# Optimization experiments

Measured on AMD Instinct MI355X. Metric: run time of the kernel, lower is better.

Reference implementation:

```python
import jax, jax.numpy as jnp
import numpy as np

THRESHOLD1 = 1.0
THRESHOLD2 = 1.0


def _conv(x, w, stride, pad):
    return jax.lax.conv_general_dilated(
        x, w, window_strides=(stride, stride),
        padding=((pad, pad), (pad, pad)),
        dimension_numbers=('NCHW', 'OIHW', 'NCHW'))


def _percentiles_1_to_99(t):
    # Faithful to torch: k = 1 + round(0.01*q*(n-1)); kthvalue = k-th smallest.
    # One sort + static gather replaces 99 kthvalue calls.
    flat = jnp.sort(t.reshape(-1))
    n = flat.shape[0]  # static under jit
    ks = np.array([1 + round(0.01 * q * (n - 1)) for q in range(1, 100)], dtype=np.int64)
    return flat[ks - 1]  # [99]


def setup_inputs() -> dict:
    key = jax.random.key(0)
    k1, k2, k3, k4 = jax.random.split(key, 4)
    x = jax.random.normal(k1, (64, 128, 56, 56), jnp.float32)
    # Kaiming-ish scaled conv weights
    w1 = jax.random.normal(k2, (256, 128, 3, 3), jnp.float32) * (2.0 / (128 * 9)) ** 0.5
    w2 = jax.random.normal(k3, (256, 256, 3, 3), jnp.float32) * (2.0 / (256 * 9)) ** 0.5
    w_id = jax.random.normal(k4, (256, 128, 1, 1), jnp.float32) * (2.0 / 128) ** 0.5
    return {"x": x, "w1": w1, "w2": w2, "w_id": w_id}


def reference(x, w1, w2, w_id):
    out1 = _conv(x, w1, 2, 1)                 # conv1: [64,256,28,28]
    a = _percentiles_1_to_99(out1)            # percentiles of UNclamped conv1 output
    out = jnp.clip(out1, 0.0, THRESHOLD1)     # out[out>t1]=t1; out[out<0]=0
    # dropout(p=0.0 / eval) is identity
    out = _conv(out, w2, 1, 1)                # conv2
    out = out + _conv(x, w_id, 2, 0)          # residual via 1x1 stride-2 downsample
    b = _percentiles_1_to_99(out)             # percentiles before second clamp
    out = jnp.clip(out, 0.0, THRESHOLD2)
    return out, a, b
```

## Files before the change

kernel.cpp:

```cpp
#include <hip/hip_runtime.h>

typedef unsigned short ushort_t;
typedef unsigned int uint_t;

using short8 = __attribute__((ext_vector_type(8))) short;
using f32x4  = __attribute__((ext_vector_type(4))) float;

#define N_BATCH   64
#define C_MID     256
#define H_OUT     28
#define W_OUT     28
#define SPATIAL   (H_OUT*W_OUT)
#define OUT_ELEMS (N_BATCH*C_MID*SPATIAL)

#define NBINS 2048
#define BIN_LO (-16.0f)
#define BIN_INV 64.0f
#define BIN_W  0.015625f

#define XT_ROW   (57*128)
#define XT_IMG   (57*57*128)
#define O1_ROW   (30*256)
#define O1_IMG   (30*30*256)

#define WAITVM(n) asm volatile("s_waitcnt vmcnt(" #n ")" ::: "memory")
#define BARRIER() asm volatile("s_barrier" ::: "memory")

__device__ __forceinline__ ushort_t f2bf(float f) {
    uint_t u = __float_as_uint(f);
    u += 0x7FFFu + ((u >> 16) & 1u);
    return (ushort_t)(u >> 16);
}

__device__ __forceinline__ void gll16(const ushort_t* g, void* l) {
    __builtin_amdgcn_global_load_lds(
        (const __attribute__((address_space(1))) unsigned int*)g,
        (__attribute__((address_space(3))) unsigned int*)l, 16, 0, 0);
}

__global__ __launch_bounds__(256) void zwtrans(
    uint_t* __restrict__ xT32, uint_t* __restrict__ o1T32,
    const float* __restrict__ w1, const float* __restrict__ w2,
    const float* __restrict__ wid, ushort_t* __restrict__ wT1,
    ushort_t* __restrict__ wT2, uint_t* __restrict__ hfA,
    uint_t* __restrict__ hfB)
{
    const int bxx = blockIdx.x, y = blockIdx.y, tid = threadIdx.x;
    if (bxx < 87) {
        int i = bxx * 256 + tid;
        int n = y;
        if (i >= 22080) return;
        if (i < 7232) {
            uint_t* base = xT32 + (size_t)n * (XT_IMG / 2);
            if (i < 3648) base[i] = 0;
            else { int j = i - 3648; int r = (j >> 6) + 1;
                   base[r * (XT_ROW / 2) + (j & 63)] = 0; }
        } else {
            int k = i - 7232;
            uint_t* base = o1T32 + (size_t)n * (O1_IMG / 2);
            if (k < 3840) base[k] = 0;
            else if (k < 7680) base[29 * (O1_ROW / 2) + (k - 3840)] = 0;
            else if (k < 11264) { int j = k - 7680; int r = (j >> 7) + 1;
                   base[r * (O1_ROW / 2) + (j & 127)] = 0; }
            else { int j = k - 11264; int r = (j >> 7) + 1;
                   base[r * (O1_ROW / 2) + 29 * 128 + (j & 127)] = 0; }
        }
    } else {
        int idx = ((bxx - 87) * 64 + y) * 256 + tid;
        if (idx < 2048)      hfA[idx] = 0;
        else if (idx < 4096) hfB[idx - 2048] = 0;
        if (idx < 256 * 1152) {
            int co = idx / 1152, k = idx % 1152;
            int g = k >> 7, ci = k & 127;
            wT1[idx] = f2bf(w1[(co * 128 + ci) * 9 + g]);
        }
        if (idx < 256 * 2432) {
            int co = idx / 2432, k = idx % 2432;
            float v;
            if (k < 2304) { int g = k >> 8, ci = k & 255; v = w2[(co * 256 + ci) * 9 + g]; }
            else          { v = wid[co * 128 + (k - 2304)]; }
            wT2[idx] = f2bf(v);
        }
    }
}

__global__ __launch_bounds__(256) void xtrans(
    const float* __restrict__ x, ushort_t* __restrict__ xT)
{
    __shared__ ushort_t t[224 * 130];
    const int tid = threadIdx.x;
    const int g = blockIdx.x, n = blockIdx.y;
    const float* xs = x + ((size_t)n * 128) * 3136 + g * 4 * 56;

    #pragma unroll
    for (int it = 0; it < 28; ++it) {
        int f = it * 256 + tid;
        int ci = f / 56, r4 = f % 56;
        float4 v = *(const float4*)(xs + ci * 3136 + r4 * 4);
        t[(r4 * 4 + 0) * 130 + ci] = f2bf(v.x);
        t[(r4 * 4 + 1) * 130 + ci] = f2bf(v.y);
        t[(r4 * 4 + 2) * 130 + ci] = f2bf(v.z);
        t[(r4 * 4 + 3) * 130 + ci] = f2bf(v.w);
    }
    __syncthreads();
    ushort_t* xo = xT + (size_t)n * XT_IMG + (g * 4 + 1) * XT_ROW + 128;
    for (int it = 0; it < 56; ++it) {
        int f = it * 256 + tid;
        int pos = f >> 6, c2 = f & 63;
        int r = pos / 56, iw = pos % 56;
        uint_t v = *(const uint_t*)&t[pos * 130 + c2 * 2];
        *(uint_t*)(xo + r * XT_ROW + iw * 128 + c2 * 2) = v;
    }
}

__global__ __launch_bounds__(256, 2) void conv1_mfma(
    const ushort_t* __restrict__ xT, const ushort_t* __restrict__ wT1,
    ushort_t* __restrict__ o1T, ushort_t* __restrict__ bh)
{
    const int bx = blockIdx.x;
    const int tid = threadIdx.x;
    const int wv = tid >> 6, lane = tid & 63;
    const int ln = lane & 15, quad = lane >> 4;
    const int n = bx / 7, rg = bx % 7, r0 = rg * 4;

    __shared__ short8 Ald[2 * 1024];
    __shared__ short8 Bp[2304];

    f32x4 acc[4][7];
    #pragma unroll
    for (int a = 0; a < 4; ++a)
        #pragma unroll
        for (int b = 0; b < 7; ++b) acc[a][b] = (f32x4){0.f, 0.f, 0.f, 0.f};

    int drb[7], cl0[7];
    #pragma unroll
    for (int b = 0; b < 7; ++b) {
        int p = b * 16 + ln;
        drb[b] = 2 * (p / 28);
        cl0[b] = p % 28;
    }

    uint_t poff[9];
    #pragma unroll
    for (int i = 0; i < 9; ++i) {
        int slot = (i * 4 + wv) * 64 + lane;
        int s2 = min(slot, 2051);
        int k8 = s2 / 513;
        int rem = s2 - k8 * 513;
        int dr = rem / 57, j = rem - dr * 57;
        int col = (j < 29) ? (2 * j) : (2 * (j - 29) + 1);
        poff[i] = (uint_t)((2 * r0 + dr) * XT_ROW + col * 128 + k8 * 8);
    }
    const uint_t aoff = (uint_t)((wv * 64 + lane) * 1152);

    const ushort_t* xTimg = xT + (size_t)n * XT_IMG;

    auto stageA = [&](int tap, int c, int buf) {
        #pragma unroll
        for (int jj = 0; jj < 4; ++jj)
            gll16(wT1 + aoff + jj * 8 + tap * 128 + c * 32,
                  (char*)Ald + buf * 16384 + (jj * 256 + wv * 64) * 16);
    };

    for (int c = 0; c < 4; ++c) {
        BARRIER();
        #pragma unroll
        for (int i = 0; i < 9; ++i)
            gll16(xTimg + poff[i] + c * 32, (char*)Bp + ((i * 4 + wv) * 64) * 16);
        if (c == 0) stageA(0, 0, 0);
        WAITVM(0);
        BARRIER();

        #pragma unroll
        for (int t = 0; t < 9; ++t) {
            const int st = c * 9 + t;
            const int buf = st & 1;
            if (t < 8)      stageA(t + 1, c, buf ^ 1);
            else if (c < 3) stageA(0, c + 1, buf ^ 1);
            if (c == 3 && t == 8) { WAITVM(0); } else { WAITVM(4); }
            const int kh = t / 3, kw = t - kh * 3;
            short8 af[4], bf[7];
            #pragma unroll
            for (int a = 0; a < 4; ++a)
                af[a] = Ald[buf * 1024 + quad * 256 + wv * 64 + a * 16 + ln];
            #pragma unroll
            for (int b = 0; b < 7; ++b) {
                int dr = drb[b] + kh;
                int j = (kw == 1) ? (29 + cl0[b]) : (cl0[b] + (kw >> 1));
                bf[b] = Bp[quad * 513 + dr * 57 + j];
            }
            __builtin_amdgcn_s_setprio(1);
            #pragma unroll
            for (int a = 0; a < 4; ++a)
                #pragma unroll
                for (int b = 0; b < 7; ++b)
                    acc[a][b] = __builtin_amdgcn_mfma_f32_16x16x32_bf16(
                        af[a], bf[b], acc[a][b], 0, 0, 0);
            __builtin_amdgcn_s_setprio(0);
        }
    }

    __syncthreads();
    uint_t* hist = (uint_t*)Ald;
    for (int i = tid; i < NBINS; i += 256) hist[i] = 0;
    __syncthreads();

    ushort_t* oimg = o1T + (size_t)n * O1_IMG;
    #pragma unroll
    for (int a = 0; a < 4; ++a) {
        int co = wv * 64 + a * 16 + quad * 4;
        #pragma unroll
        for (int b = 0; b < 7; ++b) {
            int p = b * 16 + ln;
            int h = r0 + p / 28, w = p % 28;
            ushort_t pk[4];
            #pragma unroll
            for (int r = 0; r < 4; ++r) {
                float v = acc[a][b][r];
                int bin = (int)((v - BIN_LO) * BIN_INV);
                bin = min(max(bin, 0), NBINS - 1);
                atomicAdd(&hist[bin], 1u);
                pk[r] = f2bf(fminf(fmaxf(v, 0.f), 1.f));
            }
            uint2 u; u.x = (uint_t)pk[0] | ((uint_t)pk[1] << 16);
            u.y = (uint_t)pk[2] | ((uint_t)pk[3] << 16);
            *(uint2*)(oimg + ((h + 1) * 30 + (w + 1)) * 256 + co) = u;
        }
    }

    __syncthreads();
    size_t blin = (size_t)bx * NBINS;
    for (int i = tid; i < NBINS; i += 256) bh[blin + i] = (ushort_t)hist[i];
}

__global__ __launch_bounds__(256, 2) void conv2_mfma(
    const ushort_t* __restrict__ o1T, const ushort_t* __restrict__ xT,
    const ushort_t* __restrict__ wT2, float* __restrict__ fout,
    ushort_t* __restrict__ bh)
{
    const int bx = blockIdx.x;
    const int tid = threadIdx.x;
    const int wv = tid >> 6, lane = tid & 63;
    const int ln = lane & 15, quad = lane >> 4;
    const int n = bx / 7, rg = bx % 7, r0 = rg * 4;

    __shared__ short8 Ald[2 * 1024];
    __shared__ short8 Bp[768];

    f32x4 acc[4][7];
    #pragma unroll
    for (int a = 0; a < 4; ++a)
        #pragma unroll
        for (int b = 0; b < 7; ++b) acc[a][b] = (f32x4){0.f, 0.f, 0.f, 0.f};

    int rwb[7], cl0[7];
    #pragma unroll
    for (int b = 0; b < 7; ++b) {
        int p = b * 16 + ln;
        rwb[b] = (p / 28) * 32;
        cl0[b] = p % 28;
    }

    uint_t po[3];
    #pragma unroll
    for (int jj = 0; jj < 3; ++jj) {
        int f = (wv * 3 + jj) * 64 + lane;
        int ci8 = f / 192, rem = f % 192;
        int dr = rem >> 5, cl = rem & 31;
        po[jj] = (uint_t)((r0 + dr) * O1_ROW + cl * 256 + ci8 * 8);
    }
    uint_t io[2];
    int isl[2];
    #pragma unroll
    for (int jj = 0; jj < 2; ++jj) {
        int i2 = min(wv * 2 + jj, 6);
        isl[jj] = i2;
        int slot = i2 * 64 + lane;
        int ci8 = slot / 112, pos = slot % 112;
        int h = r0 + pos / 28, w = pos % 28;
        io[jj] = (uint_t)(((2 * h + 1) * 57 + (2 * w + 1)) * 128 + ci8 * 8);
    }
    const ushort_t* asrc = wT2 + (size_t)(wv * 64 + lane) * 2432;

    const ushort_t* o1img = o1T + (size_t)n * O1_IMG;
    const ushort_t* xTimg = xT + (size_t)n * XT_IMG;

    auto stageA = [&](int k0, int buf) {
        #pragma unroll
        for (int jj = 0; jj < 4; ++jj)
            gll16(asrc + k0 + jj * 8,
                  (char*)Ald + buf * 16384 + (jj * 256 + wv * 64) * 16);
    };
    auto stageB = [&](int coff) {
        #pragma unroll
        for (int jj = 0; jj < 3; ++jj)
            gll16(o1img + po[jj] + coff, (char*)Bp + (wv * 3 + jj) * 1024);
    };
    auto stageI = [&](int idh) {
        #pragma unroll
        for (int jj = 0; jj < 2; ++jj)
            gll16(xTimg + io[jj] + idh * 32, (char*)Bp + isl[jj] * 1024);
    };

    for (int c = 0; c < 8; ++c) {
        BARRIER();
        stageB(c * 32);
        if (c == 0) stageA(0, 0);
        WAITVM(0);
        BARRIER();

        #pragma unroll
        for (int t = 0; t < 9; ++t) {
            const int st = c * 9 + t;
            const int buf = st & 1;
            if (t < 8)      stageA((t + 1) * 256 + c * 32, buf ^ 1);
            else if (c < 7) stageA(c * 32 + 32, buf ^ 1);
            if (c == 7 && t == 8) { WAITVM(0); } else { WAITVM(4); }
            const int kh = t / 3, kw = t - kh * 3;
            short8 af[4], bf[7];
            #pragma unroll
            for (int a = 0; a < 4; ++a)
                af[a] = Ald[buf * 1024 + quad * 256 + wv * 64 + a * 16 + ln];
            #pragma unroll
            for (int b = 0; b < 7; ++b)
                bf[b] = Bp[quad * 192 + rwb[b] + kh * 32 + cl0[b] + kw];
            __builtin_amdgcn_s_setprio(1);
            #pragma unroll
            for (int a = 0; a < 4; ++a)
                #pragma unroll
                for (int b = 0; b < 7; ++b)
                    acc[a][b] = __builtin_amdgcn_mfma_f32_16x16x32_bf16(
                        af[a], bf[b], acc[a][b], 0, 0, 0);
            __builtin_amdgcn_s_setprio(0);
        }
    }

    #pragma unroll
    for (int idh = 0; idh < 4; ++idh) {
        BARRIER();
        stageI(idh);
        if (idh == 0) stageA(2304, 0);
        WAITVM(0);
        BARRIER();
        if (idh < 3) stageA(2304 + (idh + 1) * 32, (idh + 1) & 1);
        short8 af[4], bf[7];
        #pragma unroll
        for (int a = 0; a < 4; ++a)
            af[a] = Ald[(idh & 1) * 1024 + quad * 256 + wv * 64 + a * 16 + ln];
        #pragma unroll
        for (int b = 0; b < 7; ++b)
            bf[b] = Bp[quad * 112 + b * 16 + ln];
        __builtin_amdgcn_s_setprio(1);
        #pragma unroll
        for (int a = 0; a < 4; ++a)
            #pragma unroll
            for (int b = 0; b < 7; ++b)
                acc[a][b] = __builtin_amdgcn_mfma_f32_16x16x32_bf16(
                    af[a], bf[b], acc[a][b], 0, 0, 0);
        __builtin_amdgcn_s_setprio(0);
    }

    __syncthreads();
    uint_t* hist = (uint_t*)Ald;
    for (int i = tid; i < NBINS; i += 256) hist[i] = 0;
    __syncthreads();

    #pragma unroll
    for (int a = 0; a < 4; ++a) {
        int co = wv * 64 + a * 16 + quad * 4;
        #pragma unroll
        for (int b = 0; b < 7; ++b) {
            int p = b * 16 + ln;
            int h = r0 + p / 28, w = p % 28;
            #pragma unroll
            for (int r = 0; r < 4; ++r) {
                float v = acc[a][b][r];
                int bin = (int)((v - BIN_LO) * BIN_INV);
                bin = min(max(bin, 0), NBINS - 1);
                atomicAdd(&hist[bin], 1u);
                fout[((size_t)(n * 256 + co + r)) * SPATIAL +
                     h * 28 + w] = fminf(fmaxf(v, 0.f), 1.f);
            }
        }
    }

    __syncthreads();
    size_t blin = (size_t)bx * NBINS;
    for (int i = tid; i < NBINS; i += 256) bh[blin + i] = (ushort_t)hist[i];
}

__global__ __launch_bounds__(256) void hreduce(
    const ushort_t* __restrict__ bhA, const ushort_t* __restrict__ bhB,
    uint_t* __restrict__ hfA, uint_t* __restrict__ hfB)
{
    const ushort_t* bh = blockIdx.z ? bhB : bhA;
    uint_t* hf = blockIdx.z ? hfB : hfA;
    const int nblk = 448;
    __shared__ uint_t p[256];
    int b0 = blockIdx.x * 64;
    int binl = threadIdx.x & 63, grp = threadIdx.x >> 6;
    int rpb = (nblk + 7) / 8;
    int j0 = blockIdx.y * rpb;
    int j1 = min(j0 + rpb, nblk);
    uint_t s = 0;
    for (int j = j0 + grp; j < j1; j += 4) s += bh[(size_t)j * NBINS + b0 + binl];
    p[threadIdx.x] = s;
    __syncthreads();
    if (threadIdx.x < 64)
        atomicAdd(&hf[b0 + threadIdx.x],
                  p[threadIdx.x] + p[64 + threadIdx.x] +
                  p[128 + threadIdx.x] + p[192 + threadIdx.x]);
}

__global__ __launch_bounds__(1024) void select_k(
    const uint_t* __restrict__ hfA, const uint_t* __restrict__ hfB,
    float* __restrict__ outp)
{
    const uint_t* hf = blockIdx.x ? hfB : hfA;
    float* op = outp + blockIdx.x * 99;
    __shared__ uint_t cs[1024];
    int t = threadIdx.x;
    uint_t s = hf[2 * t] + hf[2 * t + 1];
    cs[t] = s;
    __syncthreads();
    for (int d = 1; d < 1024; d <<= 1) {
        uint_t v = (t >= d) ? cs[t - d] : 0;
        __syncthreads();
        cs[t] += v;
        __syncthreads();
    }
    if (t >= 1 && t <= 99) {
        long long k = 1 + (long long)llrint(0.01 * (double)t * (double)(OUT_ELEMS - 1));
        int lo = 0, hi = 1023;
        while (lo < hi) { int mid = (lo + hi) >> 1; if ((long long)cs[mid] < k) lo = mid + 1; else hi = mid; }
        long long cum = (lo == 0) ? 0 : (long long)cs[lo - 1];
        int b = lo * 2;
        while (cum + (long long)hf[b] < k) { cum += hf[b]; ++b; }
        op[t - 1] = BIN_LO + ((float)b + 0.5f) * BIN_W;
    }
}

extern "C" void kernel_launch(void* const* d_in, const int* in_sizes, int n_in,
                              void* d_out, int out_size, void* d_ws, size_t ws_size,
                              hipStream_t stream)
{
    const float* x   = (const float*)d_in[0];
    const float* w1  = (const float*)d_in[1];
    const float* w2  = (const float*)d_in[2];
    const float* wid = (const float*)d_in[3];
    float* out = (float*)d_out;

    char* ws = (char*)d_ws;
    ushort_t* xT  = (ushort_t*)ws;
    ushort_t* o1T = (ushort_t*)(ws + 53235712);
    ushort_t* wT1 = (ushort_t*)(ws + 82731008);
    ushort_t* wT2 = (ushort_t*)(ws + 83320832);
    ushort_t* bhA = (ushort_t*)(ws + 84566016);
    ushort_t* bhB = (ushort_t*)(ws + 86401024);
    uint_t*   hfA = (uint_t*)  (ws + 88498176);
    uint_t*   hfB = (uint_t*)  (ws + 88506368);

    zwtrans<<<dim3(125, 64), 256, 0, stream>>>((uint_t*)xT, (uint_t*)o1T,
                                               w1, w2, wid, wT1, wT2, hfA, hfB);
    xtrans<<<dim3(14, 64), 256, 0, stream>>>(x, xT);

    conv1_mfma<<<448, 256, 0, stream>>>(xT, wT1, o1T, bhA);
    conv2_mfma<<<448, 256, 0, stream>>>(o1T, xT, wT2, out, bhB);

    hreduce<<<dim3(32, 8, 2), 256, 0, stream>>>(bhA, bhB, hfA, hfB);
    select_k<<<2, 1024, 0, stream>>>(hfA, hfB, out + OUT_ELEMS);
}
```

Baseline: 358.3 us.

## Load conv weights directly into registers and fuse histogram reduction via atomics

Both conv kernels stop staging the weight (A) operand through LDS with global_load_lds. Each lane now loads its fragments straight from global memory into double-buffered registers (af0/af1), and the loops are unrolled in pairs so buffer selection is static. This drops the LDS traffic and waits for A, at the cost of more VGPRs and more scattered global loads. Per-block histograms are now added with global atomics into the final bins, which removes the per-block histogram buffers and the separate hreduce kernel launch but adds atomic contention on 2048 bins.

```diff
diff --git a/kernel.cpp b/kernel.cpp
--- a/kernel.cpp
+++ b/kernel.cpp
@@ -37,6 +37,8 @@
         (const __attribute__((address_space(1))) unsigned int*)g,
         (__attribute__((address_space(3))) unsigned int*)l, 16, 0, 0);
 }
+
+#define AF(T, P) ((((T) + (P)) & 1) ? af1 : af0)
 
 __global__ __launch_bounds__(256) void zwtrans(
     uint_t* __restrict__ xT32, uint_t* __restrict__ o1T32,
@@ -115,7 +117,7 @@
 
 __global__ __launch_bounds__(256, 2) void conv1_mfma(
     const ushort_t* __restrict__ xT, const ushort_t* __restrict__ wT1,
-    ushort_t* __restrict__ o1T, ushort_t* __restrict__ bh)
+    ushort_t* __restrict__ o1T, uint_t* __restrict__ hf)
 {
     const int bx = blockIdx.x;
     const int tid = threadIdx.x;
@@ -123,7 +125,6 @@
     const int ln = lane & 15, quad = lane >> 4;
     const int n = bx / 7, rg = bx % 7, r0 = rg * 4;
 
-    __shared__ short8 Ald[2 * 1024];
     __shared__ short8 Bp[2304];
 
     f32x4 acc[4][7];
@@ -151,57 +152,59 @@
         int col = (j < 29) ? (2 * j) : (2 * (j - 29) + 1);
         poff[i] = (uint_t)((2 * r0 + dr) * XT_ROW + col * 128 + k8 * 8);
     }
-    const uint_t aoff = (uint_t)((wv * 64 + lane) * 1152);
+    const ushort_t* agA = wT1 + (size_t)(wv * 64 + ln) * 1152 + quad * 8;
 
     const ushort_t* xTimg = xT + (size_t)n * XT_IMG;
 
-    auto stageA = [&](int tap, int c, int buf) {
-        #pragma unroll
-        for (int jj = 0; jj < 4; ++jj)
-            gll16(wT1 + aoff + jj * 8 + tap * 128 + c * 32,
-                  (char*)Ald + buf * 16384 + (jj * 256 + wv * 64) * 16);
-    };
-
-    for (int c = 0; c < 4; ++c) {
-        BARRIER();
-        #pragma unroll
-        for (int i = 0; i < 9; ++i)
-            gll16(xTimg + poff[i] + c * 32, (char*)Bp + ((i * 4 + wv) * 64) * 16);
-        if (c == 0) stageA(0, 0, 0);
-        WAITVM(0);
-        BARRIER();
-
-        #pragma unroll
-        for (int t = 0; t < 9; ++t) {
-            const int st = c * 9 + t;
-            const int buf = st & 1;
-            if (t < 8)      stageA(t + 1, c, buf ^ 1);
-            else if (c < 3) stageA(0, c + 1, buf ^ 1);
-            if (c == 3 && t == 8) { WAITVM(0); } else { WAITVM(4); }
-            const int kh = t / 3, kw = t - kh * 3;
-            short8 af[4], bf[7];
-            #pragma unroll
-            for (int a = 0; a < 4; ++a)
-                af[a] = Ald[buf * 1024 + quad * 256 + wv * 64 + a * 16 + ln];
-            #pragma unroll
-            for (int b = 0; b < 7; ++b) {
-                int dr = drb[b] + kh;
-                int j = (kw == 1) ? (29 + cl0[b]) : (cl0[b] + (kw >> 1));
-                bf[b] = Bp[quad * 513 + dr * 57 + j];
-            }
-            __builtin_amdgcn_s_setprio(1);
-            #pragma unroll
-            for (int a = 0; a < 4; ++a)
-                #pragma unroll
-                for (int b = 0; b < 7; ++b)
-                    acc[a][b] = __builtin_amdgcn_mfma_f32_16x16x32_bf16(
-                        af[a], bf[b], acc[a][b], 0, 0, 0);
-            __builtin_amdgcn_s_setprio(0);
-        }
-    }
-
-    __syncthreads();
-    uint_t* hist = (uint_t*)Ald;
+    short8 af0[4], af1[4];
+
+#define C1_LOADA(DST, TAP, CH)                                                \
+    { _Pragma("unroll")                                                       \
+      for (int a_ = 0; a_ < 4; ++a_)                                          \
+          DST[a_] = *(const short8*)(agA + (size_t)a_ * (16 * 1152) +         \
+                                     (TAP) * 128 + (CH) * 32); }
+
+#define C1_CHUNK(C, P) do {                                                   \
+    BARRIER();                                                                \
+    _Pragma("unroll")                                                         \
+    for (int i_ = 0; i_ < 9; ++i_)                                            \
+        gll16(xTimg + poff[i_] + (C) * 32,                                    \
+              (char*)Bp + ((i_ * 4 + wv) * 64) * 16);                         \
+    if ((C) == 0) C1_LOADA(af0, 0, 0);                                        \
+    WAITVM(0);                                                                \
+    BARRIER();                                                                \
+    _Pragma("unroll")                                                         \
+    for (int t = 0; t < 9; ++t) {                                             \
+        if (t < 8)        C1_LOADA(AF(t + 1, P), t + 1, (C))                  \
+        else if ((C) < 3) C1_LOADA(AF(t + 1, P), 0, (C) + 1)                  \
+        const int kh = t / 3, kw = t - kh * 3;                                \
+        short8 bf[7];                                                         \
+        _Pragma("unroll")                                                     \
+        for (int b = 0; b < 7; ++b) {                                         \
+            int dr = drb[b] + kh;                                             \
+            int j = (kw == 1) ? (29 + cl0[b]) : (cl0[b] + (kw >> 1));         \
+            bf[b] = Bp[quad * 513 + dr * 57 + j];                             \
+        }                                                                     \
+        __builtin_amdgcn_s_setprio(1);                                        \
+        _Pragma("unroll")                                                     \
+        for (int a = 0; a < 4; ++a)                                           \
+            _Pragma("unroll")                                                 \
+            for (int b = 0; b < 7; ++b)                                       \
+                acc[a][b] = __builtin_amdgcn_mfma_f32_16x16x32_bf16(          \
+                    AF(t, P)[a], bf[b], acc[a][b], 0, 0, 0);                  \
+        __builtin_amdgcn_s_setprio(0);                                        \
+    }                                                                         \
+} while (0)
+
+    for (int c2 = 0; c2 < 2; ++c2) {
+        C1_CHUNK(2 * c2, 0);
+        C1_CHUNK(2 * c2 + 1, 1);
+    }
+#undef C1_CHUNK
+#undef C1_LOADA
+
+    __syncthreads();
+    uint_t* hist = (uint_t*)Bp;
     for (int i = tid; i < NBINS; i += 256) hist[i] = 0;
     __syncthreads();
 
@@ -229,14 +232,16 @@
     }
 
     __syncthreads();
-    size_t blin = (size_t)bx * NBINS;
-    for (int i = tid; i < NBINS; i += 256) bh[blin + i] = (ushort_t)hist[i];
+    for (int i = tid; i < NBINS; i += 256) {
+        uint_t v = hist[i];
+        if (v) atomicAdd(&hf[i], v);
+    }
 }
 
 __global__ __launch_bounds__(256, 2) void conv2_mfma(
     const ushort_t* __restrict__ o1T, const ushort_t* __restrict__ xT,
     const ushort_t* __restrict__ wT2, float* __restrict__ fout,
-    ushort_t* __restrict__ bh)
+    uint_t* __restrict__ hf)
 {
     const int bx = blockIdx.x;
     const int tid = threadIdx.x;
@@ -244,7 +249,6 @@
     const int ln = lane & 15, quad = lane >> 4;
     const int n = bx / 7, rg = bx % 7, r0 = rg * 4;
 
-    __shared__ short8 Ald[2 * 1024];
     __shared__ short8 Bp[768];
 
     f32x4 acc[4][7];
@@ -280,73 +284,63 @@
         int h = r0 + pos / 28, w = pos % 28;
         io[jj] = (uint_t)(((2 * h + 1) * 57 + (2 * w + 1)) * 128 + ci8 * 8);
     }
-    const ushort_t* asrc = wT2 + (size_t)(wv * 64 + lane) * 2432;
+    const ushort_t* agA = wT2 + (size_t)(wv * 64 + ln) * 2432 + quad * 8;
 
     const ushort_t* o1img = o1T + (size_t)n * O1_IMG;
     const ushort_t* xTimg = xT + (size_t)n * XT_IMG;
 
-    auto stageA = [&](int k0, int buf) {
-        #pragma unroll
-        for (int jj = 0; jj < 4; ++jj)
-            gll16(asrc + k0 + jj * 8,
-                  (char*)Ald + buf * 16384 + (jj * 256 + wv * 64) * 16);
-    };
-    auto stageB = [&](int coff) {
-        #pragma unroll
-        for (int jj = 0; jj < 3; ++jj)
-            gll16(o1img + po[jj] + coff, (char*)Bp + (wv * 3 + jj) * 1024);
-    };
-    auto stageI = [&](int idh) {
+    short8 af0[4], af1[4];
+
+#define C2_LOADA(DST, K)                                                      \
+    { _Pragma("unroll")                                                       \
+      for (int a_ = 0; a_ < 4; ++a_)                                          \
+          DST[a_] = *(const short8*)(agA + (size_t)a_ * (16 * 2432) + (K)); }
+
+#define C2_CHUNK(C, P) do {                                                   \
+    BARRIER();                                                                \
+    _Pragma("unroll")                                                         \
+    for (int jj = 0; jj < 3; ++jj)                                            \
+        gll16(o1img + po[jj] + (C) * 32, (char*)Bp + (wv * 3 + jj) * 1024);   \
+    if ((C) == 0) C2_LOADA(af0, 0);                                           \
+    WAITVM(0);                                                                \
+    BARRIER();                                                                \
+    _Pragma("unroll")                                                         \
+    for (int t = 0; t < 9; ++t) {                                             \
+        if (t < 8)        C2_LOADA(AF(t + 1, P), (t + 1) * 256 + (C) * 32)    \
+        else if ((C) < 7) C2_LOADA(AF(t + 1, P), ((C) + 1) * 32)              \
+        else              C2_LOADA(AF(t + 1, P), 2304)                        \
+        const int kh = t / 3, kw = t - kh * 3;                                \
+        short8 bf[7];                                                         \
+        _Pragma("unroll")                                                     \
+        for (int b = 0; b < 7; ++b)                                           \
+            bf[b] = Bp[quad * 192 + rwb[b] + kh * 32 + cl0[b] + kw];          \
+        __builtin_amdgcn_s_setprio(1);                                        \
+        _Pragma("unroll")                                                     \
+        for (int a = 0; a < 4; ++a)                                           \
+            _Pragma("unroll")                                                 \
+            for (int b = 0; b < 7; ++b)                                       \
+                acc[a][b] = __builtin_amdgcn_mfma_f32_16x16x32_bf16(          \
+                    AF(t, P)[a], bf[b], acc[a][b], 0, 0, 0);                  \
+        __builtin_amdgcn_s_setprio(0);                                        \
+    }                                                                         \
+} while (0)
+
+    for (int c2 = 0; c2 < 4; ++c2) {
+        C2_CHUNK(2 * c2, 0);
+        C2_CHUNK(2 * c2 + 1, 1);
+    }
+#undef C2_CHUNK
+
+    #pragma unroll
+    for (int idh = 0; idh < 4; ++idh) {
+        BARRIER();
         #pragma unroll
         for (int jj = 0; jj < 2; ++jj)
             gll16(xTimg + io[jj] + idh * 32, (char*)Bp + isl[jj] * 1024);
-    };
-
-    for (int c = 0; c < 8; ++c) {
-        BARRIER();
-        stageB(c * 32);
-        if (c == 0) stageA(0, 0);
         WAITVM(0);
         BARRIER();
-
-        #pragma unroll
-        for (int t = 0; t < 9; ++t) {
-            const int st = c * 9 + t;
-            const int buf = st & 1;
-            if (t < 8)      stageA((t + 1) * 256 + c * 32, buf ^ 1);
-            else if (c < 7) stageA(c * 32 + 32, buf ^ 1);
-            if (c == 7 && t == 8) { WAITVM(0); } else { WAITVM(4); }
-            const int kh = t / 3, kw = t - kh * 3;
-            short8 af[4], bf[7];
-            #pragma unroll
-            for (int a = 0; a < 4; ++a)
-                af[a] = Ald[buf * 1024 + quad * 256 + wv * 64 + a * 16 + ln];
-            #pragma unroll
-            for (int b = 0; b < 7; ++b)
-                bf[b] = Bp[quad * 192 + rwb[b] + kh * 32 + cl0[b] + kw];
-            __builtin_amdgcn_s_setprio(1);
-            #pragma unroll
-            for (int a = 0; a < 4; ++a)
-                #pragma unroll
-                for (int b = 0; b < 7; ++b)
-                    acc[a][b] = __builtin_amdgcn_mfma_f32_16x16x32_bf16(
-                        af[a], bf[b], acc[a][b], 0, 0, 0);
-            __builtin_amdgcn_s_setprio(0);
-        }
-    }
-
-    #pragma unroll
-    for (int idh = 0; idh < 4; ++idh) {
-        BARRIER();
-        stageI(idh);
-        if (idh == 0) stageA(2304, 0);
-        WAITVM(0);
-        BARRIER();
-        if (idh < 3) stageA(2304 + (idh + 1) * 32, (idh + 1) & 1);
-        short8 af[4], bf[7];
-        #pragma unroll
-        for (int a = 0; a < 4; ++a)
-            af[a] = Ald[(idh & 1) * 1024 + quad * 256 + wv * 64 + a * 16 + ln];
+        if (idh < 3) C2_LOADA(AF(idh + 1, 0), 2304 + (idh + 1) * 32)
+        short8 bf[7];
         #pragma unroll
         for (int b = 0; b < 7; ++b)
             bf[b] = Bp[quad * 112 + b * 16 + ln];
@@ -356,12 +350,13 @@
             #pragma unroll
             for (int b = 0; b < 7; ++b)
                 acc[a][b] = __builtin_amdgcn_mfma_f32_16x16x32_bf16(
-                    af[a], bf[b], acc[a][b], 0, 0, 0);
+                    AF(idh, 0)[a], bf[b], acc[a][b], 0, 0, 0);
         __builtin_amdgcn_s_setprio(0);
     }
-
-    __syncthreads();
-    uint_t* hist = (uint_t*)Ald;
+#undef C2_LOADA
+
+    __syncthreads();
+    uint_t* hist = (uint_t*)Bp;
     for (int i = tid; i < NBINS; i += 256) hist[i] = 0;
     __syncthreads();
 
@@ -385,31 +380,10 @@
     }
 
     __syncthreads();
-    size_t blin = (size_t)bx * NBINS;
-    for (int i = tid; i < NBINS; i += 256) bh[blin + i] = (ushort_t)hist[i];
-}
-
-__global__ __launch_bounds__(256) void hreduce(
-    const ushort_t* __restrict__ bhA, const ushort_t* __restrict__ bhB,
-    uint_t* __restrict__ hfA, uint_t* __restrict__ hfB)
-{
-    const ushort_t* bh = blockIdx.z ? bhB : bhA;
-    uint_t* hf = blockIdx.z ? hfB : hfA;
-    const int nblk = 448;
-    __shared__ uint_t p[256];
-    int b0 = blockIdx.x * 64;
-    int binl = threadIdx.x & 63, grp = threadIdx.x >> 6;
-    int rpb = (nblk + 7) / 8;
-    int j0 = blockIdx.y * rpb;
-    int j1 = min(j0 + rpb, nblk);
-    uint_t s = 0;
-    for (int j = j0 + grp; j < j1; j += 4) s += bh[(size_t)j * NBINS + b0 + binl];
-    p[threadIdx.x] = s;
-    __syncthreads();
-    if (threadIdx.x < 64)
-        atomicAdd(&hf[b0 + threadIdx.x],
-                  p[threadIdx.x] + p[64 + threadIdx.x] +
-                  p[128 + threadIdx.x] + p[192 + threadIdx.x]);
+    for (int i = tid; i < NBINS; i += 256) {
+        uint_t v = hist[i];
+        if (v) atomicAdd(&hf[i], v);
+    }
 }
 
 __global__ __launch_bounds__(1024) void select_k(
@@ -455,8 +429,6 @@
     ushort_t* o1T = (ushort_t*)(ws + 53235712);
     ushort_t* wT1 = (ushort_t*)(ws + 82731008);
     ushort_t* wT2 = (ushort_t*)(ws + 83320832);
-    ushort_t* bhA = (ushort_t*)(ws + 84566016);
-    ushort_t* bhB = (ushort_t*)(ws + 86401024);
     uint_t*   hfA = (uint_t*)  (ws + 88498176);
     uint_t*   hfB = (uint_t*)  (ws + 88506368);
 
@@ -464,9 +436,8 @@
                                                w1, w2, wid, wT1, wT2, hfA, hfB);
     xtrans<<<dim3(14, 64), 256, 0, stream>>>(x, xT);
 
-    conv1_mfma<<<448, 256, 0, stream>>>(xT, wT1, o1T, bhA);
-    conv2_mfma<<<448, 256, 0, stream>>>(o1T, xT, wT2, out, bhB);
-
-    hreduce<<<dim3(32, 8, 2), 256, 0, stream>>>(bhA, bhB, hfA, hfB);
+    conv1_mfma<<<448, 256, 0, stream>>>(xT, wT1, o1T, hfA);
+    conv2_mfma<<<448, 256, 0, stream>>>(o1T, xT, wT2, out, hfB);
+
     select_k<<<2, 1024, 0, stream>>>(hfA, hfB, out + OUT_ELEMS);
 }
```

New measurement: 366.6 us. 1.02x slower.
